# Kernel optimization log

Hardware: AMD Instinct MI355X
Metric: run time of the kernel (lower is better)

The kernel has to match this reference:

```python
import jax, jax.numpy as jnp
import numpy as np

B, L, K = 16, 512, 30          # proteins, residues per protein, kNN neighbors
N = B * L
H, FC = 32, 3                  # h_channels, frame_channels
C = H + FC                     # fused sphere channels (35)
HEADS, AC, VC = 8, 16, 8       # heads, alpha channels (H//2), value channels (H//4)
RBF_N, POS_N = 16, 16
EF = RBF_N + POS_N

# idealized backbone atom positions (N, CA, C) in the local residue frame
IDEAL_BB = np.array([[-0.525, 1.363, 0.0], [0.0, 0.0, 0.0], [1.526, 0.0, 0.0]], dtype=np.float32)
# cartesian (x,y,z) -> real-SH l=1 ordering (y,z,x)
P_SH = np.array([[0., 1., 0.], [0., 0., 1.], [1., 0., 0.]], dtype=np.float32)


def _knn_edges(trans):
    # per-chain brute-force kNN (chains are contiguous blocks of length L)
    X = trans.reshape(B, L, 3)
    d2 = jnp.sum((X[:, :, None, :] - X[:, None, :, :]) ** 2, axis=-1)  # [B,L,L]
    d2 = d2 + jnp.eye(L, dtype=d2.dtype) * 1e9                          # exclude self
    _, idx = jax.lax.top_k(-d2, K)                                      # [B,L,K]
    off = (jnp.arange(B) * L)[:, None, None]
    src = (idx + off).reshape(-1)              # neighbor (edge_index[0])
    tgt = jnp.repeat(jnp.arange(N), K)         # center   (edge_index[1])
    return src, tgt


def _edge_rot_mat(vec):
    # rotation aligning the edge vector with the y axis (eSCN init_edge_rot_mat style)
    nx = vec / (jnp.linalg.norm(vec, axis=-1, keepdims=True) + 1e-12)
    ref = jnp.where(jnp.abs(nx[:, :1]) < 0.9,
                    jnp.array([1., 0., 0.], dtype=vec.dtype),
                    jnp.array([0., 0., 1.], dtype=vec.dtype))
    nz = jnp.cross(nx, ref)
    nz = nz / (jnp.linalg.norm(nz, axis=-1, keepdims=True) + 1e-12)
    ny = jnp.cross(nx, nz)
    ny = ny / (jnp.linalg.norm(ny, axis=-1, keepdims=True) + 1e-12)
    return jnp.stack([nz, nx, ny], axis=-2)  # [E,3,3]


def _rbf(d, d_min=0.0, d_max=20.0, count=RBF_N):
    mu = jnp.linspace(d_min, d_max, count)
    sigma = (d_max - d_min) / count
    return jnp.exp(-(((d[:, None] - mu) / sigma) ** 2))


def _pos_emb(src, tgt, num=POS_N):
    d = (src - tgt).astype(jnp.float32)
    freq = jnp.exp(jnp.arange(0, num, 2, dtype=jnp.float32) * (-np.log(10000.0) / num))
    ang = d[:, None] * freq
    return jnp.concatenate([jnp.cos(ang), jnp.sin(ang)], axis=-1)


def _forward(rots, trans, node_emb, batch, x_mask, noising_mask,
             W_alpha, a_vec, W_v, W_o, W_g, W_2):
    src, tgt = _knn_edges(trans)
    vec = trans[src] - trans[tgt]
    dist = jnp.linalg.norm(vec, axis=-1)
    valid = jnp.isfinite(dist) & (dist > 1e-3)  # edge_select, applied as mask

    R = _edge_rot_mat(vec)
    P = jnp.asarray(P_SH)
    D1 = jnp.einsum('ij,ejk,lk->eil', P, R, P)  # l=1 Wigner in real-SH basis [E,3,3]

    edge_features = jnp.concatenate([_rbf(dist), _pos_emb(src, tgt)], axis=-1)  # [E,32]

    # fuse node features with backbone frame atoms and editability flag
    frame_atoms = jnp.einsum('nij,aj->nai', rots, jnp.asarray(IDEAL_BB))  # [N,3atoms,3xyz]
    editable = noising_mask & (~x_mask)
    emb = jnp.zeros((N, 4, C), dtype=node_emb.dtype)
    emb = emb.at[:, :, :H].set(node_emb)
    emb = emb.at[:, 1:4, H:].set(jnp.swapaxes(frame_atoms, -1, -2))
    emb = emb.at[:, 0, C - 1].set(editable.astype(node_emb.dtype))

    # gather + rotate source features into edge frames
    xs = emb[src]                                                   # [E,4,C]
    xs_rot = jnp.concatenate([xs[:, :1], jnp.einsum('eij,ejc->eic', D1, xs[:, 1:])], axis=1)

    # invariant attention logits (l=0 of rotated src, l=0 of tgt, edge feats)
    inv = jnp.concatenate([xs_rot[:, 0], emb[tgt, 0], edge_features], axis=-1)  # [E,102]
    hdn = jax.nn.silu(inv @ W_alpha).reshape(-1, HEADS, AC)
    logits = jax.nn.leaky_relu(jnp.einsum('ehk,hk->eh', hdn, a_vec), 0.2)
    logits = jnp.where(valid[:, None], logits, -1e9)

    # segment softmax over incoming edges of each target node
    mx = jax.lax.stop_gradient(jax.ops.segment_max(logits, tgt, num_segments=N))
    ex = jnp.exp(logits - mx[tgt]) * valid[:, None].astype(logits.dtype)
    den = jax.ops.segment_sum(ex, tgt, num_segments=N)
    alpha = ex / (den[tgt] + 1e-9)                                  # [E,HEADS]

    # equivariant values, attention-weighted, rotate back, scatter
    v = (xs_rot @ W_v).reshape(-1, 4, HEADS, VC)
    m = (v * alpha[:, None, :, None]).reshape(-1, 4, HEADS * VC)
    m = jnp.concatenate([m[:, :1], jnp.einsum('eji,ejc->eic', D1, m[:, 1:])], axis=1)  # D^T
    agg = jax.ops.segment_sum(m, tgt, num_segments=N)               # [N,4,64]

    y = agg @ W_o                                                    # [N,4,H]
    gate = jax.nn.silu(y[:, 0] @ W_g)                                # invariant gating FFN
    return (y * gate[:, None, :]) @ W_2                              # [N,4,H]


def setup_inputs():
    key = jax.random.key(0)
    ks = jax.random.split(key, 12)
    rots = jax.vmap(lambda m: jnp.linalg.qr(m)[0])(jax.random.normal(ks[0], (N, 3, 3)))
    trans = jax.random.normal(ks[1], (N, 3)) * 10.0
    node_emb = jax.random.normal(ks[2], (N, 4, H))
    batch = jnp.repeat(jnp.arange(B, dtype=jnp.int32), L)
    x_mask = jax.random.randint(ks[3], (N,), 0, 2).astype(bool)
    noising_mask = jax.random.randint(ks[4], (N,), 0, 2).astype(bool)
    s = lambda k, sh, fan: jax.random.normal(k, sh) / np.sqrt(fan)
    return dict(rots=rots, trans=trans, node_emb=node_emb, batch=batch,
                x_mask=x_mask, noising_mask=noising_mask,
                W_alpha=s(ks[5], (2 * C + EF, HEADS * AC), 2 * C + EF),
                a_vec=s(ks[6], (HEADS, AC), AC),
                W_v=s(ks[7], (C, HEADS * VC), C),
                W_o=s(ks[8], (HEADS * VC, H), HEADS * VC),
                W_g=s(ks[9], (H, H), H),
                W_2=s(ks[10], (H, H), H))


def reference(rots, trans, node_emb, batch, x_mask, noising_mask,
              W_alpha, a_vec, W_v, W_o, W_g, W_2):
    return _forward(rots, trans, node_emb, batch, x_mask, noising_mask,
                    W_alpha, a_vec, W_v, W_o, W_g, W_2)
```

## Files before the change

### kernel.cpp

```cpp
#include <hip/hip_runtime.h>
#include <cstdint>

#define B_ 16
#define L_ 512
#define N_ 8192
#define K_ 30
#define E_ (N_*K_)
#define H_ 32
#define C_ 35

typedef uint16_t u16;
typedef uint32_t u32;
typedef unsigned long long u64;
typedef float f2v __attribute__((ext_vector_type(2)));

static __device__ __forceinline__ f2v splat2(float x) { f2v v; v.x = x; v.y = x; return v; }

static __device__ __forceinline__ float ldf(const void* p, int i, int bf) {
    return bf ? __uint_as_float(((u32)((const u16*)p)[i]) << 16)
              : ((const float*)p)[i];
}
static __device__ __forceinline__ float bfu16(u16 x) {
    return __uint_as_float(((u32)x) << 16);
}
static __device__ __forceinline__ int ldmask(const void* p, int i, int mode) {
    if (mode == 0) return ((const unsigned char*)p)[i] != 0;
    if (mode == 2) return ((const u32*)p)[2*i] != 0;
    return ((const u32*)p)[i] != 0;
}
static __device__ __forceinline__ u16 f2bf(float f) {
    u32 x = __float_as_uint(f);
    u32 r = x + 0x7FFFu + ((x >> 16) & 1u);
    return (u16)(r >> 16);
}
static __device__ __forceinline__ float fsilu(float x) {
    return x * __builtin_amdgcn_rcpf(1.f + __expf(-x));
}

static __device__ __forceinline__ int detect_bf(const void* tr, int lane) {
    const u16* p = (const u16*)tr;
    int cnt = 0;
    for (int i = lane; i < 256; i += 64) {
        u16 v = p[2 * i];
        int e = (v >> 7) & 0xFF;
        if ((e >= 100 && e <= 141) || (v & 0x7FFFu) == 0) cnt++;
    }
    #pragma unroll
    for (int d = 1; d < 64; d <<= 1) cnt += __shfl_xor(cnt, d, 64);
    return cnt >= 192;
}
static __device__ __forceinline__ int detect_mm(const void* xmv, int lane) {
    const u32* xm = (const u32*)xmv;
    int anyBig = 0, oddNZ = 0;
    for (int i = lane; i < 1024; i += 64) {
        u32 w = xm[i];
        if (w & ~1u) anyBig = 1;
        if ((i & 1) && w) oddNZ = 1;
    }
    #pragma unroll
    for (int d = 1; d < 64; d <<= 1) {
        anyBig |= __shfl_xor(anyBig, d, 64);
        oddNZ  |= __shfl_xor(oddNZ, d, 64);
    }
    return anyBig ? 0 : (oddNZ ? 1 : 2);
}

__constant__ float cBB[9] = {-0.525f, 1.363f, 0.f,  0.f, 0.f, 0.f,  1.526f, 0.f, 0.f};

#define DPP_UMIN(var, CTRL) \
    { u32 o_ = (u32)__builtin_amdgcn_update_dpp((int)(var), (int)(var), CTRL, 0xF, 0xF, false); \
      (var) = (o_ < (var)) ? o_ : (var); }
#define DPP_UMIN_ALL(var) \
    DPP_UMIN(var, 0x111) DPP_UMIN(var, 0x112) DPP_UMIN(var, 0x114) \
    DPP_UMIN(var, 0x118) DPP_UMIN(var, 0x142) DPP_UMIN(var, 0x143)

#define DPP_ADD8(part) \
    part += __uint_as_float((u32)__builtin_amdgcn_update_dpp( \
        (int)__float_as_uint(part), (int)__float_as_uint(part), 0xB1, 0xF, 0xF, false)); \
    part += __uint_as_float((u32)__builtin_amdgcn_update_dpp( \
        (int)__float_as_uint(part), (int)__float_as_uint(part), 0x4E, 0xF, 0xF, false)); \
    part += __uint_as_float((u32)__builtin_amdgcn_update_dpp( \
        (int)__float_as_uint(part), (int)__float_as_uint(part), 0x141, 0xF, 0xF, false));

__global__ __launch_bounds__(256) void knn_kernel(const void* __restrict__ trans,
                                                  int* __restrict__ srcArr)
{
    __shared__ float sX[L_], sY[L_], sZ[L_];
    __shared__ int flagS[1];
    const int bid = blockIdx.x, tid = threadIdx.x;
    const int lane = tid & 63, wid = tid >> 6;

    if (wid == 0) {
        int bf = detect_bf(trans, lane);
        if (lane == 0) flagS[0] = bf;
    }
    __syncthreads();
    const int bf = flagS[0];
    const int t0 = bid * 4;
    const int base = (t0 >> 9) << 9;
    if (bf) {
        const u16* tp = (const u16*)trans;
        for (int i = tid; i < L_; i += 256) {
            sX[i] = bfu16(tp[(base + i) * 3 + 0]);
            sY[i] = bfu16(tp[(base + i) * 3 + 1]);
            sZ[i] = bfu16(tp[(base + i) * 3 + 2]);
        }
    } else {
        const float* tp = (const float*)trans;
        for (int i = tid; i < L_; i += 256) {
            sX[i] = tp[(base + i) * 3 + 0];
            sY[i] = tp[(base + i) * 3 + 1];
            sZ[i] = tp[(base + i) * 3 + 2];
        }
    }
    __syncthreads();

    const int t = t0 + wid;
    const int l = t & 511;
    const float tx = sX[l], ty = sY[l], tz = sZ[l];

    u32 d2b[8];
    #pragma unroll
    for (int i = 0; i < 8; ++i) {
        int j = lane + (i << 6);
        float dx = __fsub_rn(tx, sX[j]);
        float dy = __fsub_rn(ty, sY[j]);
        float dz = __fsub_rn(tz, sZ[j]);
        float d2 = __fadd_rn(__fadd_rn(__fmul_rn(dx, dx), __fmul_rn(dy, dy)), __fmul_rn(dz, dz));
        if (j == l) d2 = __fadd_rn(d2, 1e9f);
        d2b[i] = __float_as_uint(d2);
    }

    int myres = 0;
    for (int k = 0; k < K_; ++k) {
        u32 bb = d2b[0]; int bs = 0;
        #pragma unroll
        for (int i = 1; i < 8; ++i)
            if (d2b[i] < bb) { bb = d2b[i]; bs = i; }
        u32 m = bb;
        DPP_UMIN_ALL(m)
        u32 gbits = (u32)__builtin_amdgcn_readlane((int)m, 63);
        u64 mask = __ballot(bb == gbits);
        u32 gidx;
        if (__popcll(mask) == 1) {
            int wl = __ffsll((long long)mask) - 1;
            gidx = (u32)__builtin_amdgcn_readlane((int)((bs << 6) | lane), wl);
        } else {
            u32 cand = (bb == gbits) ? (u32)((bs << 6) | lane) : 0xFFFFFFFFu;
            DPP_UMIN_ALL(cand)
            gidx = (u32)__builtin_amdgcn_readlane((int)cand, 63);
        }
        if (lane == (u32)k) myres = (int)(gidx & 511u);
        if ((gidx & 63u) == (u32)lane) {
            int ws = (int)(gidx >> 6);
            #pragma unroll
            for (int i = 0; i < 8; ++i)
                if (ws == i) d2b[i] = 0xFFFFFFFFu;
        }
    }
    if (lane < K_) srcArr[t * K_ + lane] = base + myres;
}

__global__ __launch_bounds__(256) void prep_kernel(
    const void* __restrict__ rots, const void* __restrict__ trans,
    const void* __restrict__ node, const void* __restrict__ xm,
    const void* __restrict__ nm,
    const void* __restrict__ Wa, const void* __restrict__ av,
    const void* __restrict__ Wv, const void* __restrict__ Wo,
    const void* __restrict__ Wg, const void* __restrict__ W2,
    int* __restrict__ flag,
    float* __restrict__ hsrc, float* __restrict__ htgt,
    float* __restrict__ ptab, float* __restrict__ V,
    float* __restrict__ c_wrb, float* __restrict__ c_av,
    float* __restrict__ c_Wo, float* __restrict__ c_Wg, float* __restrict__ c_W2)
{
    __shared__ float eS[140];
    __shared__ int flagS[2];
    const int bid = blockIdx.x, tid = threadIdx.x;
    const int lane = tid & 63, wid = tid >> 6;

    if (bid < 8192) {
        const int n = bid;
        if (wid == 0) {
            int bf = detect_bf(trans, lane);
            int mm = detect_mm(xm, lane);
            if (lane == 0) { flagS[0] = bf; flagS[1] = mm; }
        }
        __syncthreads();
        const int bf = flagS[0], mm = flagS[1];
        if (tid < 140) {
            int r = tid / 35, c = tid - r * 35;
            float v;
            if (c < H_) {
                v = ldf(node, n * 128 + r * 32 + c, bf);
            } else if (r == 0) {
                v = (c == 34) ? ((ldmask(nm, n, mm) && !ldmask(xm, n, mm)) ? 1.f : 0.f) : 0.f;
            } else {
                int i = r - 1, a = c - 32;
                v = ldf(rots, n*9 + i*3 + 0, bf) * cBB[a*3 + 0]
                  + ldf(rots, n*9 + i*3 + 1, bf) * cBB[a*3 + 1]
                  + ldf(rots, n*9 + i*3 + 2, bf) * cBB[a*3 + 2];
            }
            eS[tid] = v;
        }
        __syncthreads();
        const int r = tid >> 6, cc = tid & 63;
        if (bf) {
            const u16* wa = (const u16*)Wa;
            const u16* wv = (const u16*)Wv;
            if (tid < 128) {
                float a = 0.f, b = 0.f;
                #pragma unroll 5
                for (int i = 0; i < 35; ++i) {
                    float v = eS[i];
                    a = fmaf(v, bfu16(wa[i * 128 + tid]),        a);
                    b = fmaf(v, bfu16(wa[(35 + i) * 128 + tid]), b);
                }
                hsrc[(size_t)n * 128 + tid] = a;
                htgt[(size_t)n * 128 + tid] = b;
            }
            const float* er = eS + r * 35;
            float acc = 0.f;
            #pragma unroll 5
            for (int cp = 0; cp < 35; ++cp) acc = fmaf(er[cp], bfu16(wv[cp * 64 + cc]), acc);
            V[(size_t)n * 256 + tid] = acc;
        } else {
            const float* wa = (const float*)Wa;
            const float* wv = (const float*)Wv;
            if (tid < 128) {
                float a = 0.f, b = 0.f;
                #pragma unroll 5
                for (int i = 0; i < 35; ++i) {
                    float v = eS[i];
                    a = fmaf(v, wa[i * 128 + tid],        a);
                    b = fmaf(v, wa[(35 + i) * 128 + tid], b);
                }
                hsrc[(size_t)n * 128 + tid] = a;
                htgt[(size_t)n * 128 + tid] = b;
            }
            const float* er = eS + r * 35;
            float acc = 0.f;
            #pragma unroll 5
            for (int cp = 0; cp < 35; ++cp) acc = fmaf(er[cp], wv[cp * 64 + cc], acc);
            V[(size_t)n * 256 + tid] = acc;
        }

    } else if (bid < 9216) {
        const int d = bid - 8192;
        if (wid == 0) {
            int bf = detect_bf(trans, lane);
            if (lane == 0) flagS[0] = bf;
        }
        __syncthreads();
        const int bf = flagS[0];
        if (tid < 128) {
            float dd = (float)(d - 512);
            float acc = 0.f;
            if (bf) {
                const u16* wa = (const u16*)Wa;
                #pragma unroll
                for (int q = 0; q < 8; ++q) {
                    float fr = expf((float)(2 * q) * (-0.5756462732485115f));
                    float ang = dd * fr;
                    acc = fmaf(cosf(ang), bfu16(wa[(86 + q) * 128 + tid]), acc);
                    acc = fmaf(sinf(ang), bfu16(wa[(94 + q) * 128 + tid]), acc);
                }
            } else {
                const float* wa = (const float*)Wa;
                #pragma unroll
                for (int q = 0; q < 8; ++q) {
                    float fr = expf((float)(2 * q) * (-0.5756462732485115f));
                    float ang = dd * fr;
                    acc = fmaf(cosf(ang), wa[(86 + q) * 128 + tid], acc);
                    acc = fmaf(sinf(ang), wa[(94 + q) * 128 + tid], acc);
                }
            }
            ptab[(size_t)d * 128 + tid] = acc;
        }

    } else {
        if (wid == 0) {
            int bf = detect_bf(trans, lane);
            if (lane == 0) flagS[0] = bf;
        }
        __syncthreads();
        const int bf = flagS[0];
        if (bid == 9216 && tid == 0) flag[0] = bf;
        int g0 = (bid - 9216) * 256 + tid;
        for (int i = g0; i < 6272; i += 2048) {
            if      (i < 2048) c_wrb[i]        = ldf(Wa, 70 * 128 + i, bf);
            else if (i < 2176) c_av[i - 2048]  = ldf(av, i - 2048, bf);
            else if (i < 4224) c_Wo[i - 2176]  = ldf(Wo, i - 2176, bf);
            else if (i < 5248) c_Wg[i - 4224]  = ldf(Wg, i - 4224, bf);
            else               c_W2[i - 5248]  = ldf(W2, i - 5248, bf);
        }
    }
}

__global__ __launch_bounds__(128) void logits_kernel(
    const void* __restrict__ trans, const int* __restrict__ srcArr,
    const float* __restrict__ hsrc, const float* __restrict__ htgt,
    const float* __restrict__ ptab,
    const float* __restrict__ c_wrb, const float* __restrict__ c_av,
    const int* __restrict__ flag, float* __restrict__ logitsw)
{
    __shared__ float rbfS[2][32][20];
    __shared__ int   srcS[2][32];
    __shared__ int   tgtS[2][32];
    __shared__ int   dS[2][32];
    __shared__ float lgS[2][256];
    const int tid = threadIdx.x, wid = tid >> 6, lane = tid & 63;
    const int bf = flag[0];

    const f2v* cw = (const f2v*)c_wrb;
    const f2v w0 = cw[0*64+lane],  w1 = cw[1*64+lane],  w2 = cw[2*64+lane],  w3 = cw[3*64+lane];
    const f2v w4 = cw[4*64+lane],  w5 = cw[5*64+lane],  w6 = cw[6*64+lane],  w7 = cw[7*64+lane];
    const f2v w8 = cw[8*64+lane],  w9 = cw[9*64+lane],  wA = cw[10*64+lane], wB = cw[11*64+lane];
    const f2v wC = cw[12*64+lane], wD = cw[13*64+lane], wE = cw[14*64+lane], wF = cw[15*64+lane];
    const f2v avv = ((const f2v*)c_av)[lane];

    const int e0 = (blockIdx.x * 2 + wid) * 32;

    {
        const int el  = lane & 31;
        const int e   = e0 + el;
        const int tgt = e / K_;
        int src = srcArr[e];
        src = (src < 0) ? 0 : ((src >= N_) ? (N_ - 1) : src);
        float vx = ldf(trans, src*3+0, bf) - ldf(trans, tgt*3+0, bf);
        float vy = ldf(trans, src*3+1, bf) - ldf(trans, tgt*3+1, bf);
        float vz = ldf(trans, src*3+2, bf) - ldf(trans, tgt*3+2, bf);
        float dist = sqrtf(vx*vx + vy*vy + vz*vz);
        bool valid = isfinite(dist) && (dist > 1e-3f);
        int d = src - tgt + 512;
        d = (d < 0) ? 0 : ((d > 1023) ? 1023 : d);
        if (lane < 32) {
            srcS[wid][el] = src;
            tgtS[wid][el] = tgt;
            dS[wid][el]   = d | (valid ? 0 : (1 << 16));
        }
        const int jb = (lane >> 5) * 8;
        #pragma unroll
        for (int j = 0; j < 8; ++j) {
            float tt = (dist - (float)(jb + j) * (20.f/15.f)) * 0.8f;
            rbfS[wid][el][jb + j] = __expf(-tt * tt);
        }
    }
    __syncthreads();

    const float* hsL = hsrc + (lane << 1);
    const float* htL = htgt + (lane << 1);
    const float* ptL = ptab + (lane << 1);
    #pragma unroll 2
    for (int q = 0; q < 32; ++q) {
        const int src = srcS[wid][q];
        const int tgt = tgtS[wid][q];
        const int dm  = dS[wid][q];
        const int d   = dm & 0xFFFF;
        const bool valid = (dm >> 16) == 0;

        f2v hs = *(const f2v*)(hsL + (src << 7));
        f2v ht = *(const f2v*)(htL + (tgt << 7));
        f2v pt = *(const f2v*)(ptL + (d << 7));
        f2v acc = (hs + ht) + pt;
        const float4* rp = (const float4*)(&rbfS[wid][q][0]);
        float4 ra = rp[0], rb = rp[1], rc = rp[2], rd = rp[3];
        acc = __builtin_elementwise_fma(splat2(ra.x), w0, acc);
        acc = __builtin_elementwise_fma(splat2(ra.y), w1, acc);
        acc = __builtin_elementwise_fma(splat2(ra.z), w2, acc);
        acc = __builtin_elementwise_fma(splat2(ra.w), w3, acc);
        acc = __builtin_elementwise_fma(splat2(rb.x), w4, acc);
        acc = __builtin_elementwise_fma(splat2(rb.y), w5, acc);
        acc = __builtin_elementwise_fma(splat2(rb.z), w6, acc);
        acc = __builtin_elementwise_fma(splat2(rb.w), w7, acc);
        acc = __builtin_elementwise_fma(splat2(rc.x), w8, acc);
        acc = __builtin_elementwise_fma(splat2(rc.y), w9, acc);
        acc = __builtin_elementwise_fma(splat2(rc.z), wA, acc);
        acc = __builtin_elementwise_fma(splat2(rc.w), wB, acc);
        acc = __builtin_elementwise_fma(splat2(rd.x), wC, acc);
        acc = __builtin_elementwise_fma(splat2(rd.y), wD, acc);
        acc = __builtin_elementwise_fma(splat2(rd.z), wE, acc);
        acc = __builtin_elementwise_fma(splat2(rd.w), wF, acc);
        float part = fsilu(acc.x) * avv.x + fsilu(acc.y) * avv.y;
        DPP_ADD8(part)
        float lg = (part >= 0.f) ? part : 0.2f * part;
        if (!valid) lg = -1e9f;
        lg = (fabsf(lg) < 1e30f) ? lg : -1e9f;
        if ((lane & 7) == 0) lgS[wid][q * 8 + (lane >> 3)] = lg;
    }
    __syncthreads();
    {
        float4* dst = (float4*)(logitsw + (size_t)e0 * 8);
        dst[lane] = ((const float4*)lgS[wid])[lane];
    }
}

__global__ __launch_bounds__(256) void agg_out_kernel(
    const float* __restrict__ V, const int* __restrict__ srcArr,
    const float* __restrict__ logitsw,
    const float* __restrict__ Wo, const float* __restrict__ Wg,
    const float* __restrict__ W2,
    const int* __restrict__ flag, void* __restrict__ outv)
{
    __shared__ float lgS[240];
    __shared__ float invS[8];
    __shared__ int   voffS[K_];
    __shared__ float aggS[256];
    __shared__ float ybuf[128];
    __shared__ float gbuf[32];
    const int bid = blockIdx.x, tid = threadIdx.x;
    const int t   = ((bid & 7) << 10) | (bid >> 3);
    const int bf = flag[0];

    if (tid < 240) lgS[tid] = logitsw[(size_t)t * 240 + tid];
    if (tid < K_) {
        int s = srcArr[t * K_ + tid];
        s = (s < 0) ? 0 : ((s >= N_) ? (N_ - 1) : s);
        voffS[tid] = s << 8;
    }
    __syncthreads();

    if (tid < 8) {
        float mx = -1e30f;
        #pragma unroll
        for (int k = 0; k < K_; ++k) mx = fmaxf(mx, lgS[k * 8 + tid]);
        float den = 0.f;
        #pragma unroll
        for (int k = 0; k < K_; ++k) {
            float l = lgS[k * 8 + tid];
            float e = (l > -1e8f) ? __expf(l - mx) : 0.f;
            lgS[k * 8 + tid] = e; den += e;
        }
        invS[tid] = 1.f / (den + 1e-9f);
    }
    __syncthreads();

    {
        const int h = (tid & 63) >> 3;
        float vv[K_];
        #pragma unroll
        for (int k = 0; k < K_; ++k) vv[k] = V[voffS[k] + tid];
        float acc = 0.f;
        #pragma unroll
        for (int k = 0; k < K_; ++k) acc = fmaf(lgS[k * 8 + h], vv[k], acc);
        aggS[tid] = acc * invS[h];
    }
    __syncthreads();

    if (tid < 128) {
        int rr = tid >> 5, o = tid & 31;
        float y = 0.f;
        #pragma unroll
        for (int c = 0; c < 64; ++c) y = fmaf(aggS[rr * 64 + c], Wo[c * 32 + o], y);
        ybuf[tid] = y;
    }
    __syncthreads();
    if (tid < 32) {
        float g = 0.f;
        #pragma unroll
        for (int o = 0; o < 32; ++o) g = fmaf(ybuf[o], Wg[o * 32 + tid], g);
        gbuf[tid] = fsilu(g);
    }
    __syncthreads();
    if (tid < 128) {
        int rr = tid >> 5, hh = tid & 31;
        float o = 0.f;
        #pragma unroll
        for (int g = 0; g < 32; ++g) o = fmaf(ybuf[rr * 32 + g] * gbuf[g], W2[g * 32 + hh], o);
        o = (fabsf(o) < 1e30f) ? o : 0.f;
        size_t idx = (size_t)t * 128 + tid;
        if (bf) ((u16*)outv)[idx] = f2bf(o);
        else    ((float*)outv)[idx] = o;
    }
}

extern "C" void kernel_launch(void* const* d_in, const int* in_sizes, int n_in,
                              void* d_out, int out_size, void* d_ws, size_t ws_size,
                              hipStream_t stream)
{
    const void* rots         = d_in[0];
    const void* trans        = d_in[1];
    const void* node_emb     = d_in[2];
    const void* x_mask       = d_in[4];
    const void* noising_mask = d_in[5];
    const void* Wa           = d_in[6];
    const void* avec         = d_in[7];
    const void* Wv           = d_in[8];
    const void* Wo           = d_in[9];
    const void* Wg           = d_in[10];
    const void* W2           = d_in[11];

    char* ws = (char*)d_ws;
    int*   flag    = (int*)  (ws + 0);
    int*   srcArr  = (int*)  (ws + 64);
    float* hsrc    = (float*)(ws + 983104);
    float* htgt    = (float*)(ws + 5177408);
    float* ptab    = (float*)(ws + 9371712);
    float* V       = (float*)(ws + 9896000);
    float* c_wrb   = (float*)(ws + 18284608);
    float* c_av    = (float*)(ws + 18292800);
    float* c_Wo    = (float*)(ws + 18293312);
    float* c_Wg    = (float*)(ws + 18301504);
    float* c_W2    = (float*)(ws + 18305600);
    float* logitsw = (float*)(ws + 18309696);

    hipLaunchKernelGGL(knn_kernel, dim3(N_/4), dim3(256), 0, stream, trans, srcArr);
    hipLaunchKernelGGL(prep_kernel, dim3(8192 + 1024 + 8), dim3(256), 0, stream,
                       rots, trans, node_emb, x_mask, noising_mask,
                       Wa, avec, Wv, Wo, Wg, W2,
                       flag, hsrc, htgt, ptab, V,
                       c_wrb, c_av, c_Wo, c_Wg, c_W2);
    hipLaunchKernelGGL(logits_kernel, dim3(E_/64), dim3(128), 0, stream,
                       trans, srcArr, hsrc, htgt, ptab, c_wrb, c_av, flag, logitsw);
    hipLaunchKernelGGL(agg_out_kernel, dim3(N_), dim3(256), 0, stream,
                       V, srcArr, logitsw, c_Wo, c_Wg, c_W2, flag, d_out);
}
```

Measured before the change: 217.5 us.

## Restructure prep kernel to one wave per node with readlane broadcasts

Moves dtype/mask-mode detection into block 0 of the kNN kernel, which writes global flags, so prep blocks no longer each rerun detection or hit a block barrier. Prep now maps one wavefront per node (4 nodes per block) and holds the 140 fused-sphere values in registers, broadcasting them with readlane instead of going through shared memory. The position table packs two rows per block. This cuts the block count and removes redundant detection and syncs, at the cost of more register pressure and a fully unrolled loop.

```diff
diff --git a/kernel.cpp b/kernel.cpp
--- a/kernel.cpp
+++ b/kernel.cpp
@@ -36,6 +36,9 @@
 static __device__ __forceinline__ float fsilu(float x) {
     return x * __builtin_amdgcn_rcpf(1.f + __expf(-x));
 }
+static __device__ __forceinline__ float RL(float x, int i) {
+    return __uint_as_float((u32)__builtin_amdgcn_readlane((int)__float_as_uint(x), i));
+}
 
 static __device__ __forceinline__ int detect_bf(const void* tr, int lane) {
     const u16* p = (const u16*)tr;
@@ -83,6 +86,8 @@
         (int)__float_as_uint(part), (int)__float_as_uint(part), 0x141, 0xF, 0xF, false));
 
 __global__ __launch_bounds__(256) void knn_kernel(const void* __restrict__ trans,
+                                                  const void* __restrict__ xm,
+                                                  int* __restrict__ flag,
                                                   int* __restrict__ srcArr)
 {
     __shared__ float sX[L_], sY[L_], sZ[L_];
@@ -92,6 +97,10 @@
 
     if (wid == 0) {
         int bf = detect_bf(trans, lane);
+        if (bid == 0) {
+            int mm = detect_mm(xm, lane);
+            if (lane == 0) { flag[0] = bf; flag[1] = mm; }
+        }
         if (lane == 0) flagS[0] = bf;
     }
     __syncthreads();
@@ -162,131 +171,138 @@
 }
 
 __global__ __launch_bounds__(256) void prep_kernel(
-    const void* __restrict__ rots, const void* __restrict__ trans,
-    const void* __restrict__ node, const void* __restrict__ xm,
-    const void* __restrict__ nm,
+    const void* __restrict__ rots, const void* __restrict__ node,
+    const void* __restrict__ xm, const void* __restrict__ nm,
     const void* __restrict__ Wa, const void* __restrict__ av,
     const void* __restrict__ Wv, const void* __restrict__ Wo,
     const void* __restrict__ Wg, const void* __restrict__ W2,
-    int* __restrict__ flag,
+    const int* __restrict__ flag,
     float* __restrict__ hsrc, float* __restrict__ htgt,
     float* __restrict__ ptab, float* __restrict__ V,
     float* __restrict__ c_wrb, float* __restrict__ c_av,
     float* __restrict__ c_Wo, float* __restrict__ c_Wg, float* __restrict__ c_W2)
 {
-    __shared__ float eS[140];
-    __shared__ int flagS[2];
     const int bid = blockIdx.x, tid = threadIdx.x;
     const int lane = tid & 63, wid = tid >> 6;
-
-    if (bid < 8192) {
-        const int n = bid;
-        if (wid == 0) {
-            int bf = detect_bf(trans, lane);
-            int mm = detect_mm(xm, lane);
-            if (lane == 0) { flagS[0] = bf; flagS[1] = mm; }
-        }
-        __syncthreads();
-        const int bf = flagS[0], mm = flagS[1];
-        if (tid < 140) {
-            int r = tid / 35, c = tid - r * 35;
-            float v;
-            if (c < H_) {
-                v = ldf(node, n * 128 + r * 32 + c, bf);
-            } else if (r == 0) {
-                v = (c == 34) ? ((ldmask(nm, n, mm) && !ldmask(xm, n, mm)) ? 1.f : 0.f) : 0.f;
-            } else {
+    const int bf = flag[0], mm = flag[1];
+
+    if (bid < 2048) {
+        const int n = bid * 4 + wid;
+
+        float eA, eB, eC = 0.f;
+        {
+            int s = lane;
+            int r = s / 35, c = s - r * 35;
+            if (c < H_)      eA = ldf(node, n * 128 + r * 32 + c, bf);
+            else if (r == 0) eA = (c == 34) ? ((ldmask(nm, n, mm) && !ldmask(xm, n, mm)) ? 1.f : 0.f) : 0.f;
+            else {
                 int i = r - 1, a = c - 32;
-                v = ldf(rots, n*9 + i*3 + 0, bf) * cBB[a*3 + 0]
-                  + ldf(rots, n*9 + i*3 + 1, bf) * cBB[a*3 + 1]
-                  + ldf(rots, n*9 + i*3 + 2, bf) * cBB[a*3 + 2];
-            }
-            eS[tid] = v;
-        }
-        __syncthreads();
-        const int r = tid >> 6, cc = tid & 63;
+                eA = ldf(rots, n*9 + i*3 + 0, bf) * cBB[a*3 + 0]
+                   + ldf(rots, n*9 + i*3 + 1, bf) * cBB[a*3 + 1]
+                   + ldf(rots, n*9 + i*3 + 2, bf) * cBB[a*3 + 2];
+            }
+            s = lane + 64;
+            r = s / 35; c = s - r * 35;
+            if (c < H_)      eB = ldf(node, n * 128 + r * 32 + c, bf);
+            else {
+                int i = r - 1, a = c - 32;
+                eB = ldf(rots, n*9 + i*3 + 0, bf) * cBB[a*3 + 0]
+                   + ldf(rots, n*9 + i*3 + 1, bf) * cBB[a*3 + 1]
+                   + ldf(rots, n*9 + i*3 + 2, bf) * cBB[a*3 + 2];
+            }
+            if (lane < 12) {
+                s = lane + 128;
+                r = s / 35; c = s - r * 35;
+                if (c < H_)      eC = ldf(node, n * 128 + r * 32 + c, bf);
+                else {
+                    int i = r - 1, a = c - 32;
+                    eC = ldf(rots, n*9 + i*3 + 0, bf) * cBB[a*3 + 0]
+                       + ldf(rots, n*9 + i*3 + 1, bf) * cBB[a*3 + 1]
+                       + ldf(rots, n*9 + i*3 + 2, bf) * cBB[a*3 + 2];
+                }
+            }
+        }
+
+        float a0 = 0.f, a1 = 0.f, b0 = 0.f, b1 = 0.f;
+        float v0 = 0.f, v1 = 0.f, v2 = 0.f, v3 = 0.f;
         if (bf) {
             const u16* wa = (const u16*)Wa;
             const u16* wv = (const u16*)Wv;
-            if (tid < 128) {
-                float a = 0.f, b = 0.f;
-                #pragma unroll 5
-                for (int i = 0; i < 35; ++i) {
-                    float v = eS[i];
-                    a = fmaf(v, bfu16(wa[i * 128 + tid]),        a);
-                    b = fmaf(v, bfu16(wa[(35 + i) * 128 + tid]), b);
-                }
-                hsrc[(size_t)n * 128 + tid] = a;
-                htgt[(size_t)n * 128 + tid] = b;
-            }
-            const float* er = eS + r * 35;
-            float acc = 0.f;
-            #pragma unroll 5
-            for (int cp = 0; cp < 35; ++cp) acc = fmaf(er[cp], bfu16(wv[cp * 64 + cc]), acc);
-            V[(size_t)n * 256 + tid] = acc;
+            #pragma unroll
+            for (int i = 0; i < 35; ++i) {
+                float ei = RL(eA, i);
+                a0 = fmaf(ei, bfu16(wa[i * 128 + lane]),        a0);
+                a1 = fmaf(ei, bfu16(wa[i * 128 + lane + 64]),   a1);
+                b0 = fmaf(ei, bfu16(wa[(35 + i) * 128 + lane]),      b0);
+                b1 = fmaf(ei, bfu16(wa[(35 + i) * 128 + lane + 64]), b1);
+            }
+            #pragma unroll
+            for (int cp = 0; cp < 35; ++cp) {
+                float w = bfu16(wv[cp * 64 + lane]);
+                float e1 = (35 + cp < 64) ? RL(eA, 35 + cp) : RL(eB, cp - 29);
+                float e3 = (cp < 23) ? RL(eB, 41 + cp) : RL(eC, cp - 23);
+                v0 = fmaf(RL(eA, cp), w, v0);
+                v1 = fmaf(e1, w, v1);
+                v2 = fmaf(RL(eB, cp + 6), w, v2);
+                v3 = fmaf(e3, w, v3);
+            }
         } else {
             const float* wa = (const float*)Wa;
             const float* wv = (const float*)Wv;
-            if (tid < 128) {
-                float a = 0.f, b = 0.f;
-                #pragma unroll 5
-                for (int i = 0; i < 35; ++i) {
-                    float v = eS[i];
-                    a = fmaf(v, wa[i * 128 + tid],        a);
-                    b = fmaf(v, wa[(35 + i) * 128 + tid], b);
-                }
-                hsrc[(size_t)n * 128 + tid] = a;
-                htgt[(size_t)n * 128 + tid] = b;
-            }
-            const float* er = eS + r * 35;
-            float acc = 0.f;
-            #pragma unroll 5
-            for (int cp = 0; cp < 35; ++cp) acc = fmaf(er[cp], wv[cp * 64 + cc], acc);
-            V[(size_t)n * 256 + tid] = acc;
-        }
-
-    } else if (bid < 9216) {
-        const int d = bid - 8192;
-        if (wid == 0) {
-            int bf = detect_bf(trans, lane);
-            if (lane == 0) flagS[0] = bf;
-        }
-        __syncthreads();
-        const int bf = flagS[0];
-        if (tid < 128) {
-            float dd = (float)(d - 512);
-            float acc = 0.f;
-            if (bf) {
-                const u16* wa = (const u16*)Wa;
-                #pragma unroll
-                for (int q = 0; q < 8; ++q) {
-                    float fr = expf((float)(2 * q) * (-0.5756462732485115f));
-                    float ang = dd * fr;
-                    acc = fmaf(cosf(ang), bfu16(wa[(86 + q) * 128 + tid]), acc);
-                    acc = fmaf(sinf(ang), bfu16(wa[(94 + q) * 128 + tid]), acc);
-                }
-            } else {
-                const float* wa = (const float*)Wa;
-                #pragma unroll
-                for (int q = 0; q < 8; ++q) {
-                    float fr = expf((float)(2 * q) * (-0.5756462732485115f));
-                    float ang = dd * fr;
-                    acc = fmaf(cosf(ang), wa[(86 + q) * 128 + tid], acc);
-                    acc = fmaf(sinf(ang), wa[(94 + q) * 128 + tid], acc);
-                }
-            }
-            ptab[(size_t)d * 128 + tid] = acc;
-        }
+            #pragma unroll
+            for (int i = 0; i < 35; ++i) {
+                float ei = RL(eA, i);
+                a0 = fmaf(ei, wa[i * 128 + lane],        a0);
+                a1 = fmaf(ei, wa[i * 128 + lane + 64],   a1);
+                b0 = fmaf(ei, wa[(35 + i) * 128 + lane],      b0);
+                b1 = fmaf(ei, wa[(35 + i) * 128 + lane + 64], b1);
+            }
+            #pragma unroll
+            for (int cp = 0; cp < 35; ++cp) {
+                float w = wv[cp * 64 + lane];
+                float e1 = (35 + cp < 64) ? RL(eA, 35 + cp) : RL(eB, cp - 29);
+                float e3 = (cp < 23) ? RL(eB, 41 + cp) : RL(eC, cp - 23);
+                v0 = fmaf(RL(eA, cp), w, v0);
+                v1 = fmaf(e1, w, v1);
+                v2 = fmaf(RL(eB, cp + 6), w, v2);
+                v3 = fmaf(e3, w, v3);
+            }
+        }
+        hsrc[(size_t)n * 128 + lane]      = a0;
+        hsrc[(size_t)n * 128 + lane + 64] = a1;
+        htgt[(size_t)n * 128 + lane]      = b0;
+        htgt[(size_t)n * 128 + lane + 64] = b1;
+        float* vp = V + (size_t)n * 256 + lane;
+        vp[0] = v0; vp[64] = v1; vp[128] = v2; vp[192] = v3;
+
+    } else if (bid < 2560) {
+        const int d   = (bid - 2048) * 2 + (tid >> 7);
+        const int col = tid & 127;
+        float dd = (float)(d - 512);
+        float acc = 0.f;
+        if (bf) {
+            const u16* wa = (const u16*)Wa;
+            #pragma unroll
+            for (int q = 0; q < 8; ++q) {
+                float fr = expf((float)(2 * q) * (-0.5756462732485115f));
+                float ang = dd * fr;
+                acc = fmaf(cosf(ang), bfu16(wa[(86 + q) * 128 + col]), acc);
+                acc = fmaf(sinf(ang), bfu16(wa[(94 + q) * 128 + col]), acc);
+            }
+        } else {
+            const float* wa = (const float*)Wa;
+            #pragma unroll
+            for (int q = 0; q < 8; ++q) {
+                float fr = expf((float)(2 * q) * (-0.5756462732485115f));
+                float ang = dd * fr;
+                acc = fmaf(cosf(ang), wa[(86 + q) * 128 + col], acc);
+                acc = fmaf(sinf(ang), wa[(94 + q) * 128 + col], acc);
+            }
+        }
+        ptab[(size_t)d * 128 + col] = acc;
 
     } else {
-        if (wid == 0) {
-            int bf = detect_bf(trans, lane);
-            if (lane == 0) flagS[0] = bf;
-        }
-        __syncthreads();
-        const int bf = flagS[0];
-        if (bid == 9216 && tid == 0) flag[0] = bf;
-        int g0 = (bid - 9216) * 256 + tid;
+        int g0 = (bid - 2560) * 256 + tid;
         for (int i = g0; i < 6272; i += 2048) {
             if      (i < 2048) c_wrb[i]        = ldf(Wa, 70 * 128 + i, bf);
             else if (i < 2176) c_av[i - 2048]  = ldf(av, i - 2048, bf);
@@ -504,11 +520,12 @@
     float* c_W2    = (float*)(ws + 18305600);
     float* logitsw = (float*)(ws + 18309696);
 
-    hipLaunchKernelGGL(knn_kernel, dim3(N_/4), dim3(256), 0, stream, trans, srcArr);
-    hipLaunchKernelGGL(prep_kernel, dim3(8192 + 1024 + 8), dim3(256), 0, stream,
-                       rots, trans, node_emb, x_mask, noising_mask,
-                       Wa, avec, Wv, Wo, Wg, W2,
-                       flag, hsrc, htgt, ptab, V,
+    hipLaunchKernelGGL(knn_kernel, dim3(N_/4), dim3(256), 0, stream,
+                       trans, x_mask, flag, srcArr);
+    hipLaunchKernelGGL(prep_kernel, dim3(2048 + 512 + 8), dim3(256), 0, stream,
+                       rots, node_emb, x_mask, noising_mask,
+                       Wa, avec, Wv, Wo, Wg, W2, flag,
+                       hsrc, htgt, ptab, V,
                        c_wrb, c_av, c_Wo, c_Wg, c_W2);
     hipLaunchKernelGGL(logits_kernel, dim3(E_/64), dim3(128), 0, stream,
                        trans, srcArr, hsrc, htgt, ptab, c_wrb, c_av, flag, logitsw);
```

Result: faster. 201.9 us, median of 2 (-7.2%).
